# Optimization experiments

Measured on AMD Instinct MI355X. Metric: run time of the kernel, lower is better.

The kernel has to match this reference:

```python
import jax, jax.numpy as jnp
import numpy as np

B, CIN, CMID, COUT, H, W = 4, 64, 128, 128, 128, 128
K = 9  # 3x3 taps
EPS = 1e-5


def conv3x3(x, w, b):
    # standard 3x3 conv, stride 1, pad 1, NCHW / OIHW
    y = jax.lax.conv_general_dilated(x, w, (1, 1), ((1, 1), (1, 1)),
                                     dimension_numbers=('NCHW', 'OIHW', 'NCHW'))
    return y + b[None, :, None, None]


def deform_conv3x3(x, offset, w, b):
    # torchvision DeformConv2d semantics (v1, no mask), kernel 3, pad 1, stride 1.
    # offset: [B, 2*K, H, W] with per-tap (dy, dx) pairs.
    Bn, C, Hn, Wn = x.shape
    off = offset.reshape(Bn, K, 2, Hn, Wn)
    off_y, off_x = off[:, :, 0], off[:, :, 1]          # [B,K,H,W]
    ky = (jnp.arange(K) // 3).astype(x.dtype)          # tap row 0..2
    kx = (jnp.arange(K) % 3).astype(x.dtype)           # tap col 0..2
    # sampling positions: p = out_pos - pad + tap + offset
    py = jnp.arange(Hn, dtype=x.dtype)[None, None, :, None] - 1.0 + ky[None, :, None, None] + off_y
    px = jnp.arange(Wn, dtype=x.dtype)[None, None, None, :] - 1.0 + kx[None, :, None, None] + off_x
    y0 = jnp.floor(py); x0 = jnp.floor(px)
    wy1 = py - y0; wx1 = px - x0                       # bilinear fractions
    y0i = y0.astype(jnp.int32); x0i = x0.astype(jnp.int32)
    xf = x.reshape(Bn, C, Hn * Wn)

    def gather(iy, ix):
        valid = ((iy >= 0) & (iy < Hn) & (ix >= 0) & (ix < Wn)).astype(x.dtype)
        idx = jnp.clip(iy, 0, Hn - 1) * Wn + jnp.clip(ix, 0, Wn - 1)  # [B,K,H,W]
        g = jax.vmap(lambda xb, ib: xb[:, ib])(xf, idx)               # [B,C,K,H,W]
        return g, valid

    g00, v00 = gather(y0i, x0i)
    g01, v01 = gather(y0i, x0i + 1)
    g10, v10 = gather(y0i + 1, x0i)
    g11, v11 = gather(y0i + 1, x0i + 1)

    def wmul(g, v, wgt):
        return g * (v * wgt)[:, None]                  # broadcast over channel dim

    sampled = (wmul(g00, v00, (1 - wy1) * (1 - wx1)) +
               wmul(g01, v01, (1 - wy1) * wx1) +
               wmul(g10, v10, wy1 * (1 - wx1)) +
               wmul(g11, v11, wy1 * wx1))              # [B,C,K,H,W]
    out = jnp.einsum('bckhw,ock->bohw', sampled, w.reshape(w.shape[0], C, K))
    return out + b[None, :, None, None]


def batchnorm_relu(x, gamma, beta):
    # training-mode BN: batch statistics over (N,H,W), biased variance
    mean = jnp.mean(x, axis=(0, 2, 3), keepdims=True)
    var = jnp.mean(jnp.square(x - mean), axis=(0, 2, 3), keepdims=True)
    y = (x - mean) * jax.lax.rsqrt(var + EPS)
    return jax.nn.relu(y * gamma[None, :, None, None] + beta[None, :, None, None])


def setup_inputs() -> dict:
    key = jax.random.key(0)
    ks = jax.random.split(key, 13)
    s = 0.05  # small weights keep offsets small / sampling mostly in-bounds
    return {
        'x': jax.random.normal(ks[0], (B, CIN, H, W), jnp.float32),
        'w_off1': jax.random.normal(ks[1], (2 * K, CIN, 3, 3), jnp.float32) * s,
        'b_off1': jnp.zeros((2 * K,), jnp.float32),
        'w1': jax.random.normal(ks[2], (CMID, CIN, 3, 3), jnp.float32) * s,
        'b1': jax.random.normal(ks[3], (CMID,), jnp.float32) * s,
        'g1': jnp.ones((CMID,), jnp.float32),
        'be1': jnp.zeros((CMID,), jnp.float32),
        'w_off2': jax.random.normal(ks[4], (2 * K, CMID, 3, 3), jnp.float32) * s,
        'b_off2': jnp.zeros((2 * K,), jnp.float32),
        'w2': jax.random.normal(ks[5], (COUT, CMID, 3, 3), jnp.float32) * s,
        'b2': jax.random.normal(ks[6], (COUT,), jnp.float32) * s,
        'g2': jnp.ones((COUT,), jnp.float32),
        'be2': jnp.zeros((COUT,), jnp.float32),
    }


def reference(x, w_off1, b_off1, w1, b1, g1, be1, w_off2, b_off2, w2, b2, g2, be2):
    offset1 = conv3x3(x, w_off1, b_off1)
    out = deform_conv3x3(x, offset1, w1, b1)
    out = batchnorm_relu(out, g1, be1)
    offset2 = conv3x3(out, w_off2, b_off2)
    out = deform_conv3x3(out, offset2, w2, b2)
    out = batchnorm_relu(out, g2, be2)
    return out
```

## Files before the change

kernel.cpp:

```cpp
#include <hip/hip_runtime.h>
#include <hip/hip_bf16.h>

#define BB 4
#define H_ 128
#define W_ 128
#define HWP 16384
#define CIN1 64
#define CMID 128
#define KOFF 18

typedef short short8 __attribute__((ext_vector_type(8)));
typedef float floatx4 __attribute__((ext_vector_type(4)));

#define WS_AB   16
#define WS_CVT  288
#define CVT_TOTAL 4447396
#define WS_WF1  4447744
#define WS_WF2  4484608
#define WS_XT   4558336
#define WS_OFF  6655488
#define WS_Y1   7835136
#define WS_Y1T  16223744
#define WS_OFFB 20418048
#define WS_PART 21600000
#define WS_Y2   WS_Y1

#define R_X     0
#define R_WOFF1 4194304
#define R_BOFF1 4204672
#define R_W1    4204690
#define R_B1    4278418
#define R_G1    4278546
#define R_BE1   4278674
#define R_WOFF2 4278802
#define R_BOFF2 4299538
#define R_W2    4299556
#define R_B2    4447012
#define R_G2    4447140
#define R_BE2   4447268

struct SrcPtrs { const void* p[13]; };

__device__ inline short f2bf(float f) {
    __hip_bfloat16 h = __float2bfloat16(f);
    return *reinterpret_cast<short*>(&h);
}
__device__ inline float bf2f(unsigned short u) {
    return __uint_as_float(((unsigned int)u) << 16);
}
__device__ inline float bfu_lo(unsigned int u) { return __uint_as_float(u << 16); }
__device__ inline float bfu_hi(unsigned int u) { return __uint_as_float(u & 0xFFFF0000u); }
__device__ inline float rl_f(float v, int i) {
    return __int_as_float(__builtin_amdgcn_readlane(__float_as_int(v), i));
}

__global__ void probe_dtype_k(const unsigned int* __restrict__ g1, int* __restrict__ flag) {
    if (threadIdx.x == 0 && blockIdx.x == 0) {
        flag[0] = ((g1[0] & 0xFFFFu) != 0u) ? 1 : 0;
    }
}

__global__ __launch_bounds__(256) void convert_inputs_k(SrcPtrs sp, float* __restrict__ dst,
                                                        const int* __restrict__ flag, int total) {
    int i = blockIdx.x * 256 + threadIdx.x;
    if (i >= total) return;
    constexpr int prefix[13] = {0, R_WOFF1, R_BOFF1, R_W1, R_B1, R_G1, R_BE1,
                                R_WOFF2, R_BOFF2, R_W2, R_B2, R_G2, R_BE2};
    const void* src = sp.p[0];
    int base = 0;
#pragma unroll
    for (int q = 1; q < 13; ++q) {
        if (i >= prefix[q]) { src = sp.p[q]; base = prefix[q]; }
    }
    int local = i - base;
    float v;
    if (flag[0] != 0) {
        v = bf2f(((const unsigned short*)src)[local]);
    } else {
        v = ((const float*)src)[local];
    }
    dst[i] = v;
}

template <int CIN>
__global__ __launch_bounds__(256) void wf_build_k(const float* __restrict__ w, short* __restrict__ wf) {
    constexpr int KSTEPS = CIN * 9 / 32;
    int idx = blockIdx.x * 256 + threadIdx.x;
    int j    = idx & 7;
    int lane = (idx >> 3) & 63;
    int rem  = idx >> 9;
    int ks   = rem % KSTEPS;
    int ct   = rem / KSTEPS;
    int co = ct * 16 + (lane & 15);
    int k  = ks * 32 + (lane >> 4) * 8 + j;
    int ci = k & (CIN - 1);
    int kk = k / CIN;
    wf[idx] = f2bf(w[(co * CIN + ci) * 9 + kk]);
}

__global__ __launch_bounds__(256) void xt_build_k(const float* __restrict__ x, unsigned short* __restrict__ xt) {
    __shared__ __align__(4) short s_t[64 * 66];
    int bi  = blockIdx.x;
    int hw0 = (bi & 255) * 64;
    int b   = bi >> 8;
    int t   = threadIdx.x;
    int hwp = t & 63;
#pragma unroll
    for (int it = 0; it < 16; ++it) {
        int c = it * 4 + (t >> 6);
        float v = x[((long)(b * 64 + c) << 14) + hw0 + hwp];
        s_t[hwp * 66 + c] = f2bf(v);
    }
    __syncthreads();
#pragma unroll
    for (int it = 0; it < 8; ++it) {
        int i  = it * 256 + t;
        int c2 = (i & 31) * 2;
        int hw2 = i >> 5;
        int sv = *(const int*)&s_t[hw2 * 66 + c2];
        *(int*)&xt[((long)((b << 14) + hw0 + hw2)) * 64 + c2] = sv;
    }
}

template <int CIN>
__global__ __launch_bounds__(256) void conv3x3_part_k(const float* __restrict__ x,
                                                      const float* __restrict__ w,
                                                      const float* __restrict__ bias,
                                                      float* __restrict__ outp,
                                                      float* __restrict__ outpb) {
    constexpr int CIQ = CIN / 2;
    int bi = blockIdx.x;
    int h  = bi & 127;
    int b  = (bi >> 7) & 3;
    int q  = bi >> 9;
    int t  = threadIdx.x;
    int wq = t & 127;
    int cg = __builtin_amdgcn_readfirstlane(t >> 7);
    int co0 = cg * 9;
    int ci0 = q * CIQ;

    float acc[9];
#pragma unroll
    for (int j = 0; j < 9; ++j) acc[j] = (q == 0) ? bias[co0 + j] : 0.f;

    const float* xb = x + ((long)(b * CIN + ci0) << 14);
    bool bm = h > 0, bp = h < H_ - 1, bl = wq > 0, br = wq < W_ - 1;
    int rm = (bm ? h - 1 : 0) << 7;
    int rc = h << 7;
    int rp = (bp ? h + 1 : H_ - 1) << 7;

#pragma unroll 2
    for (int ci = 0; ci < CIQ; ++ci) {
        const float* plane = xb + ((long)ci << 14);
        float v0 = plane[rm + wq - 1], v1 = plane[rm + wq], v2 = plane[rm + wq + 1];
        float v3 = plane[rc + wq - 1], v4 = plane[rc + wq], v5 = plane[rc + wq + 1];
        float v6 = plane[rp + wq - 1], v7 = plane[rp + wq], v8 = plane[rp + wq + 1];
        v0 = (bm && bl) ? v0 : 0.f;
        v1 = bm ? v1 : 0.f;
        v2 = (bm && br) ? v2 : 0.f;
        v3 = bl ? v3 : 0.f;
        v5 = br ? v5 : 0.f;
        v6 = (bp && bl) ? v6 : 0.f;
        v7 = bp ? v7 : 0.f;
        v8 = (bp && br) ? v8 : 0.f;
#pragma unroll
        for (int j = 0; j < 9; ++j) {
            const float* wk = w + ((long)(co0 + j) * CIN + ci0 + ci) * 9;
            acc[j] += v0 * wk[0] + v1 * wk[1] + v2 * wk[2]
                    + v3 * wk[3] + v4 * wk[4] + v5 * wk[5]
                    + v6 * wk[6] + v7 * wk[7] + v8 * wk[8];
        }
    }

    float* o = (q == 0) ? outp : outpb;
    long ob = ((long)(b * KOFF + co0) << 14) + (h << 7) + wq;
#pragma unroll
    for (int j = 0; j < 9; ++j) o[ob + ((long)j << 14)] = acc[j];
}

__device__ inline void build_table2(const float* __restrict__ off, const float* __restrict__ offb,
                                    int b, int h, int w0, int lane, int wv,
                                    int& tpk, float& tw0, float& tw1, float& tw2, float& tw3) {
    tpk = 0; tw0 = tw1 = tw2 = tw3 = 0.f;
    if (lane < 36) {
        int r = wv + 8 * lane;
        int p = r & 31;
        int k = r >> 5;
        int wpix = w0 + p;
        long obase = ((long)(b * KOFF) << 14) + (h << 7) + wpix;
        long oyi = obase + ((long)(2 * k) << 14);
        long oxi = obase + ((long)(2 * k + 1) << 14);
        float oy = off[oyi] + offb[oyi];
        float ox = off[oxi] + offb[oxi];
        float py = (float)(h - 1 + (k / 3)) + oy;
        float px = (float)(wpix - 1 + (k % 3)) + ox;
        float fy = floorf(py), fx = floorf(px);
        float wy = py - fy, wx = px - fx;
        int y0 = (int)fy, x0 = (int)fx;
        int y1 = y0 + 1, x1 = x0 + 1;
        bool vy0 = (y0 >= 0) && (y0 < H_);
        bool vy1 = (y1 >= 0) && (y1 < H_);
        bool vx0 = (x0 >= 0) && (x0 < W_);
        bool vx1 = (x1 >= 0) && (x1 < W_);
        float wy0 = 1.f - wy, wx0 = 1.f - wx;
        tw0 = (vy0 && vx0) ? wy0 * wx0 : 0.f;
        tw1 = (vy0 && vx1) ? wy0 * wx  : 0.f;
        tw2 = (vy1 && vx0) ? wy  * wx0 : 0.f;
        tw3 = (vy1 && vx1) ? wy  * wx  : 0.f;
        int iy0 = min(max(y0, 0), H_ - 1), iy1 = min(max(y1, 0), H_ - 1);
        int ix0 = min(max(x0, 0), W_ - 1), ix1 = min(max(x1, 0), W_ - 1);
        int dx = ix1 - ix0;
        int dy = iy1 - iy0;
        tpk = (iy0 * W_ + ix0) | (dx << 14) | (dy << 15);
    }
}

template <int NB>
__device__ inline void gather_batch128v2(const unsigned short* __restrict__ xb, short* __restrict__ s_samp,
                                         int i0, int kkbase, int wv, int lane,
                                         int tpk, float tw0, float tw1, float tw2, float tw3) {
    constexpr int PADc = 648;
    uint4 ub[NB];
#pragma unroll
    for (int j = 0; j < NB; ++j) {
        int pk = __builtin_amdgcn_readlane(tpk, i0 + j);
        const unsigned short* b00 = xb + (pk & 0x3FFF) * 128;
        const unsigned short* b01 = b00 + ((pk >> 14) & 1) * 128;
        const unsigned short* b10 = b00 + ((pk >> 15) & 1) * (W_ * 128);
        const unsigned short* b11 = b01 + ((pk >> 15) & 1) * (W_ * 128);
        ub[j].x = *(const unsigned int*)(b00 + 2 * lane);
        ub[j].y = *(const unsigned int*)(b01 + 2 * lane);
        ub[j].z = *(const unsigned int*)(b10 + 2 * lane);
        ub[j].w = *(const unsigned int*)(b11 + 2 * lane);
    }
#pragma unroll
    for (int j = 0; j < NB; ++j) {
        int i = i0 + j;
        int r = wv + 8 * i;
        float w00 = rl_f(tw0, i), w01 = rl_f(tw1, i), w10 = rl_f(tw2, i), w11 = rl_f(tw3, i);
        float vlo = w00 * bfu_lo(ub[j].x) + w01 * bfu_lo(ub[j].y)
                  + w10 * bfu_lo(ub[j].z) + w11 * bfu_lo(ub[j].w);
        float vhi = w00 * bfu_hi(ub[j].x) + w01 * bfu_hi(ub[j].y)
                  + w10 * bfu_hi(ub[j].z) + w11 * bfu_hi(ub[j].w);
        __hip_bfloat162 h2 = __float22bfloat162_rn(make_float2(vlo, vhi));
        *(unsigned int*)&s_samp[(r & 31) * PADc + ((r >> 5) - kkbase) * 128 + 2 * lane] =
            *reinterpret_cast<unsigned int*>(&h2);
    }
}

template <int NBP>
__device__ inline void gather_batch64v2(const unsigned short* __restrict__ xb, short* __restrict__ s_samp,
                                        int i0, int wv, int half, int li,
                                        int tpk, float tw0, float tw1, float tw2, float tw3) {
    constexpr int PADc = 584;
    uint4 ub[NBP];
#pragma unroll
    for (int j = 0; j < NBP; ++j) {
        int iA = i0 + 2 * j, iB = iA + 1;
        int pkA = __builtin_amdgcn_readlane(tpk, iA);
        int pkB = __builtin_amdgcn_readlane(tpk, iB);
        int pk = half ? pkB : pkA;
        const unsigned short* b00 = xb + (pk & 0x3FFF) * 64;
        const unsigned short* b01 = b00 + ((pk >> 14) & 1) * 64;
        const unsigned short* b10 = b00 + ((pk >> 15) & 1) * (W_ * 64);
        const unsigned short* b11 = b01 + ((pk >> 15) & 1) * (W_ * 64);
        ub[j].x = *(const unsigned int*)(b00 + 2 * li);
        ub[j].y = *(const unsigned int*)(b01 + 2 * li);
        ub[j].z = *(const unsigned int*)(b10 + 2 * li);
        ub[j].w = *(const unsigned int*)(b11 + 2 * li);
    }
#pragma unroll
    for (int j = 0; j < NBP; ++j) {
        int iA = i0 + 2 * j, iB = iA + 1;
        float w00 = half ? rl_f(tw0, iB) : rl_f(tw0, iA);
        float w01 = half ? rl_f(tw1, iB) : rl_f(tw1, iA);
        float w10 = half ? rl_f(tw2, iB) : rl_f(tw2, iA);
        float w11 = half ? rl_f(tw3, iB) : rl_f(tw3, iA);
        float vlo = w00 * bfu_lo(ub[j].x) + w01 * bfu_lo(ub[j].y)
                  + w10 * bfu_lo(ub[j].z) + w11 * bfu_lo(ub[j].w);
        float vhi = w00 * bfu_hi(ub[j].x) + w01 * bfu_hi(ub[j].y)
                  + w10 * bfu_hi(ub[j].z) + w11 * bfu_hi(ub[j].w);
        __hip_bfloat162 h2 = __float22bfloat162_rn(make_float2(vlo, vhi));
        int r = wv + 8 * (half ? iB : iA);
        *(unsigned int*)&s_samp[(r & 31) * PADc + (r >> 5) * 64 + 2 * li] =
            *reinterpret_cast<unsigned int*>(&h2);
    }
}

__global__ __launch_bounds__(512, 4) void deform_mfma64_k(const unsigned short* __restrict__ xt,
                                                          const float* __restrict__ off,
                                                          const float* __restrict__ offb,
                                                          const short* __restrict__ wf,
                                                          const float* __restrict__ bias,
                                                          float* __restrict__ out) {
    constexpr int KSTEPS = 18;
    constexpr int PADc = 584;
    __shared__ __align__(16) short s_samp[32 * PADc];

    int bi = blockIdx.x;
    int w0 = (bi & 3) * 32;
    int h  = (bi >> 2) & 127;
    int b  = bi >> 9;
    int t  = threadIdx.x;
    int lane = t & 63;
    int wv   = t >> 6;

    int tpk; float tw0, tw1, tw2, tw3;
    build_table2(off, offb, b, h, w0, lane, wv, tpk, tw0, tw1, tw2, tw3);
    const unsigned short* xb = xt + (long)b * HWP * 64;
    int half = lane >> 5, li = lane & 31;

    gather_batch64v2<6>(xb, s_samp,  0, wv, half, li, tpk, tw0, tw1, tw2, tw3);
    gather_batch64v2<6>(xb, s_samp, 12, wv, half, li, tpk, tw0, tw1, tw2, tw3);
    gather_batch64v2<6>(xb, s_samp, 24, wv, half, li, tpk, tw0, tw1, tw2, tw3);
    __syncthreads();

    int p_   = lane & 15;
    int quad = lane >> 4;
    int ct = wv;
    floatx4 acc0, acc1;
#pragma unroll
    for (int r = 0; r < 4; ++r) {
        float bv = bias[ct * 16 + quad * 4 + r];
        acc0[r] = bv;
        acc1[r] = bv;
    }
#pragma unroll 3
    for (int ks = 0; ks < KSTEPS; ++ks) {
        short8 a  = *(const short8*)&wf[(((long)ct * KSTEPS + ks) * 64 + lane) * 8];
        short8 b0 = *(const short8*)&s_samp[p_ * PADc + ks * 32 + quad * 8];
        short8 b1 = *(const short8*)&s_samp[(16 + p_) * PADc + ks * 32 + quad * 8];
        acc0 = __builtin_amdgcn_mfma_f32_16x16x32_bf16(a, b0, acc0, 0, 0, 0);
        acc1 = __builtin_amdgcn_mfma_f32_16x16x32_bf16(a, b1, acc1, 0, 0, 0);
    }

    long ob = ((long)(b * 128) << 14) + (h << 7) + w0 + p_;
#pragma unroll
    for (int r = 0; r < 4; ++r) {
        long cpl = (long)(ct * 16 + quad * 4 + r) << 14;
        out[ob + cpl]      = acc0[r];
        out[ob + 16 + cpl] = acc1[r];
    }
}

__global__ __launch_bounds__(512, 4) void deform_mfma128_k(const unsigned short* __restrict__ xt,
                                                           const float* __restrict__ off,
                                                           const float* __restrict__ offb,
                                                           const short* __restrict__ wf,
                                                           const float* __restrict__ bias,
                                                           float* __restrict__ out) {
    constexpr int KSTEPS = 36;
    constexpr int PADc = 648;
    __shared__ __align__(16) short s_samp[32 * PADc];

    int bi = blockIdx.x;
    int w0 = (bi & 3) * 32;
    int h  = (bi >> 2) & 127;
    int b  = bi >> 9;
    int t  = threadIdx.x;
    int lane = t & 63;
    int wv   = t >> 6;

    int tpk; float tw0, tw1, tw2, tw3;
    build_table2(off, offb, b, h, w0, lane, wv, tpk, tw0, tw1, tw2, tw3);
    const unsigned short* xb = xt + (long)b * HWP * 128;

    int p_   = lane & 15;
    int quad = lane >> 4;
    int ct = wv;
    floatx4 acc0, acc1;
#pragma unroll
    for (int r = 0; r < 4; ++r) {
        float bv = bias[ct * 16 + quad * 4 + r];
        acc0[r] = bv;
        acc1[r] = bv;
    }

    gather_batch128v2<8>(xb, s_samp, 0, 0, wv, lane, tpk, tw0, tw1, tw2, tw3);
    gather_batch128v2<8>(xb, s_samp, 8, 0, wv, lane, tpk, tw0, tw1, tw2, tw3);
    __syncthreads();
#pragma unroll 4
    for (int ks = 0; ks < 16; ++ks) {
        short8 a  = *(const short8*)&wf[(((long)ct * KSTEPS + ks) * 64 + lane) * 8];
        short8 b0 = *(const short8*)&s_samp[p_ * PADc + ks * 32 + quad * 8];
        short8 b1 = *(const short8*)&s_samp[(16 + p_) * PADc + ks * 32 + quad * 8];
        acc0 = __builtin_amdgcn_mfma_f32_16x16x32_bf16(a, b0, acc0, 0, 0, 0);
        acc1 = __builtin_amdgcn_mfma_f32_16x16x32_bf16(a, b1, acc1, 0, 0, 0);
    }
    __syncthreads();

    gather_batch128v2<5>(xb, s_samp, 16, 4, wv, lane, tpk, tw0, tw1, tw2, tw3);
    gather_batch128v2<5>(xb, s_samp, 21, 4, wv, lane, tpk, tw0, tw1, tw2, tw3);
    gather_batch128v2<5>(xb, s_samp, 26, 4, wv, lane, tpk, tw0, tw1, tw2, tw3);
    gather_batch128v2<5>(xb, s_samp, 31, 4, wv, lane, tpk, tw0, tw1, tw2, tw3);
    __syncthreads();
#pragma unroll 4
    for (int ks = 16; ks < KSTEPS; ++ks) {
        short8 a  = *(const short8*)&wf[(((long)ct * KSTEPS + ks) * 64 + lane) * 8];
        short8 b0 = *(const short8*)&s_samp[p_ * PADc + (ks - 16) * 32 + quad * 8];
        short8 b1 = *(const short8*)&s_samp[(16 + p_) * PADc + (ks - 16) * 32 + quad * 8];
        acc0 = __builtin_amdgcn_mfma_f32_16x16x32_bf16(a, b0, acc0, 0, 0, 0);
        acc1 = __builtin_amdgcn_mfma_f32_16x16x32_bf16(a, b1, acc1, 0, 0, 0);
    }

    long ob = ((long)(b * 128) << 14) + (h << 7) + w0 + p_;
#pragma unroll
    for (int r = 0; r < 4; ++r) {
        long cpl = (long)(ct * 16 + quad * 4 + r) << 14;
        out[ob + cpl]      = acc0[r];
        out[ob + 16 + cpl] = acc1[r];
    }
}

__global__ __launch_bounds__(256) void bn_stats_part_k(const float* __restrict__ y, float* __restrict__ part) {
    int bi = blockIdx.x;
    int c = bi & 127;
    int b = bi >> 7;
    int t = threadIdx.x;
    const float4* p4 = (const float4*)(y + ((long)(b * 128 + c) << 14));
    float sum = 0.f, ss = 0.f;
#pragma unroll
    for (int i = 0; i < 16; ++i) {
        float4 v = p4[t + 256 * i];
        sum += v.x + v.y + v.z + v.w;
        ss  += v.x * v.x + v.y * v.y + v.z * v.z + v.w * v.w;
    }
#pragma unroll
    for (int o = 32; o > 0; o >>= 1) { sum += __shfl_down(sum, o); ss += __shfl_down(ss, o); }
    __shared__ float s1[4], s2[4];
    int wave = t >> 6;
    if ((t & 63) == 0) { s1[wave] = sum; s2[wave] = ss; }
    __syncthreads();
    if (t == 0) {
        part[bi]       = s1[0] + s1[1] + s1[2] + s1[3];
        part[512 + bi] = s2[0] + s2[1] + s2[2] + s2[3];
    }
}

__global__ __launch_bounds__(256) void bn_apply_dual_k(float* __restrict__ y, const float* __restrict__ part,
                                                       const float* __restrict__ g, const float* __restrict__ be,
                                                       unsigned short* __restrict__ yt) {
    __shared__ __align__(4) short s_t[64 * 134];
    __shared__ float s_a[128], s_sh[128];
    int t = threadIdx.x;
    if (t < 128) {
        float sum = part[t] + part[128 + t] + part[256 + t] + part[384 + t];
        float ss  = part[512 + t] + part[640 + t] + part[768 + t] + part[896 + t];
        float mean = sum * (1.f / 65536.f);
        float var  = ss  * (1.f / 65536.f) - mean * mean;
        float inv  = rsqrtf(var + 1e-5f);
        float a = g[t] * inv;
        s_a[t]  = a;
        s_sh[t] = be[t] - mean * a;
    }
    __syncthreads();

    int bi  = blockIdx.x;
    int hw0 = (bi & 255) * 64;
    int b   = bi >> 8;
    int hwp = t & 63;
#pragma unroll 4
    for (int it = 0; it < 32; ++it) {
        int c = it * 4 + (t >> 6);
        float a = s_a[c], sh = s_sh[c];
        long addr = ((long)(b * 128 + c) << 14) + hw0 + hwp;
        float v = y[addr];
        v = fmaxf(v * a + sh, 0.f);
        y[addr] = v;
        s_t[hwp * 134 + c] = f2bf(v);
    }
    __syncthreads();
#pragma unroll 4
    for (int it = 0; it < 16; ++it) {
        int i   = it * 256 + t;
        int c2  = (i & 63) * 2;
        int hw2 = i >> 6;
        int sv = *(const int*)&s_t[hw2 * 134 + c2];
        *(int*)&yt[((long)((b << 14) + hw0 + hw2)) * 128 + c2] = sv;
    }
}

__global__ __launch_bounds__(256) void bn_apply_out_k(const float* __restrict__ y, const float* __restrict__ part,
                                                      const float* __restrict__ g, const float* __restrict__ be,
                                                      const int* __restrict__ flag, void* __restrict__ out, int total4) {
    __shared__ float s_a[128], s_sh[128];
    int t = threadIdx.x;
    if (t < 128) {
        float sum = part[t] + part[128 + t] + part[256 + t] + part[384 + t];
        float ss  = part[512 + t] + part[640 + t] + part[768 + t] + part[896 + t];
        float mean = sum * (1.f / 65536.f);
        float var  = ss  * (1.f / 65536.f) - mean * mean;
        float inv  = rsqrtf(var + 1e-5f);
        float a = g[t] * inv;
        s_a[t]  = a;
        s_sh[t] = be[t] - mean * a;
    }
    __syncthreads();

    int i = blockIdx.x * 256 + t;
    if (i >= total4) return;
    int c = (i >> 12) & 127;
    float a = s_a[c], sh = s_sh[c];
    float4 v = reinterpret_cast<const float4*>(y)[i];
    v.x = fmaxf(v.x * a + sh, 0.f);
    v.y = fmaxf(v.y * a + sh, 0.f);
    v.z = fmaxf(v.z * a + sh, 0.f);
    v.w = fmaxf(v.w * a + sh, 0.f);
    if (flag[0] != 0) {
        ushort4 u;
        u.x = (unsigned short)f2bf(v.x);
        u.y = (unsigned short)f2bf(v.y);
        u.z = (unsigned short)f2bf(v.z);
        u.w = (unsigned short)f2bf(v.w);
        reinterpret_cast<ushort4*>(out)[i] = u;
    } else {
        reinterpret_cast<float4*>(out)[i] = v;
    }
}

extern "C" void kernel_launch(void* const* d_in, const int* in_sizes, int n_in,
                              void* d_out, int out_size, void* d_ws, size_t ws_size,
                              hipStream_t stream) {
    float* ws   = (float*)d_ws;
    int*   flag = (int*)d_ws;
    float* cvt  = ws + WS_CVT;

    const float* X     = cvt + R_X;
    const float* Woff1 = cvt + R_WOFF1;
    const float* Boff1 = cvt + R_BOFF1;
    const float* W1f   = cvt + R_W1;
    const float* B1f   = cvt + R_B1;
    const float* G1    = cvt + R_G1;
    const float* Be1   = cvt + R_BE1;
    const float* Woff2 = cvt + R_WOFF2;
    const float* Boff2 = cvt + R_BOFF2;
    const float* W2f   = cvt + R_W2;
    const float* B2f   = cvt + R_B2;
    const float* G2    = cvt + R_G2;
    const float* Be2   = cvt + R_BE2;

    short* WF1 = (short*)(ws + WS_WF1);
    short* WF2 = (short*)(ws + WS_WF2);
    unsigned short* XT  = (unsigned short*)(ws + WS_XT);
    unsigned short* Y1T = (unsigned short*)(ws + WS_Y1T);
    float* OFF  = ws + WS_OFF;
    float* OFFB = ws + WS_OFFB;
    float* PART = ws + WS_PART;
    float* Y1   = ws + WS_Y1;
    float* Y2   = ws + WS_Y2;

    SrcPtrs sp;
    for (int j = 0; j < 13; ++j) sp.p[j] = d_in[j];

    probe_dtype_k<<<1, 64, 0, stream>>>((const unsigned int*)d_in[5], flag);
    convert_inputs_k<<<(CVT_TOTAL + 255) / 256, 256, 0, stream>>>(sp, cvt, flag, CVT_TOTAL);
    wf_build_k<64><<<288, 256, 0, stream>>>(W1f, WF1);
    wf_build_k<128><<<576, 256, 0, stream>>>(W2f, WF2);
    xt_build_k<<<1024, 256, 0, stream>>>(X, XT);

    conv3x3_part_k<64><<<BB * 128 * 2, 256, 0, stream>>>(X, Woff1, Boff1, OFF, OFFB);
    deform_mfma64_k<<<BB * 128 * 4, 512, 0, stream>>>(XT, OFF, OFFB, WF1, B1f, Y1);
    bn_stats_part_k<<<512, 256, 0, stream>>>(Y1, PART);
    bn_apply_dual_k<<<1024, 256, 0, stream>>>(Y1, PART, G1, Be1, Y1T);

    conv3x3_part_k<128><<<BB * 128 * 2, 256, 0, stream>>>(Y1, Woff2, Boff2, OFF, OFFB);
    deform_mfma128_k<<<BB * 128 * 4, 512, 0, stream>>>(Y1T, OFF, OFFB, WF2, B2f, Y2);
    bn_stats_part_k<<<512, 256, 0, stream>>>(Y2, PART);
    bn_apply_out_k<<<(BB * 128 * HWP / 4 + 255) / 256, 256, 0, stream>>>(Y2, PART, G2, Be2, flag, d_out, BB * 128 * HWP / 4);
}
```

Measured before the change: 335.2 us.

## Compute offset convolutions with split-bf16 MFMA instead of scalar FP32

Replaces the scalar FP32 direct offset-conv kernels with MFMA kernels that gather 3x3 neighbourhoods from the channel-last bf16 tensors into LDS. Weights and activations are each split into a bf16 hi part and a bf16 lo residual, and three MFMA products (hi*hi, lo*hi, hi*lo) approximate FP32 accuracy. The K reduction is split across waves and combined in LDS, which removes the old partial-sum buffer and the extra load in build_table2. In exchange, the builder kernels must write extra lo-residual tensors, reusing workspace regions whose old contents are assumed dead.

```diff
diff --git a/kernel.cpp b/kernel.cpp
--- a/kernel.cpp
+++ b/kernel.cpp
@@ -21,7 +21,8 @@
 #define WS_OFF  6655488
 #define WS_Y1   7835136
 #define WS_Y1T  16223744
-#define WS_OFFB 20418048
+#define WS_WFO1 20418048
+#define WS_WFO2 20436480
 #define WS_PART 21600000
 #define WS_Y2   WS_Y1
 
@@ -98,8 +99,30 @@
     wf[idx] = f2bf(w[(co * CIN + ci) * 9 + kk]);
 }
 
-__global__ __launch_bounds__(256) void xt_build_k(const float* __restrict__ x, unsigned short* __restrict__ xt) {
+template <int CIN>
+__global__ __launch_bounds__(256) void wf_off_build_k(const float* __restrict__ w, short* __restrict__ wf) {
+    constexpr int KSTEPS = CIN * 9 / 32;
+    int idx = blockIdx.x * 256 + threadIdx.x;
+    int j    = idx & 7;
+    int lane = (idx >> 3) & 63;
+    int rem  = idx >> 9;
+    int ks   = rem % KSTEPS;
+    int cc   = rem / KSTEPS;
+    int sel  = cc >> 1;
+    int co = (cc & 1) * 16 + (lane & 15);
+    int k  = ks * 32 + (lane >> 4) * 8 + j;
+    int ci = k & (CIN - 1);
+    int kk = k / CIN;
+    float v = (co < KOFF) ? w[(co * CIN + ci) * 9 + kk] : 0.f;
+    short hi = f2bf(v);
+    wf[idx] = sel ? f2bf(v - bf2f((unsigned short)hi)) : hi;
+}
+
+__global__ __launch_bounds__(256) void xt_build_k(const float* __restrict__ x,
+                                                  unsigned short* __restrict__ xt,
+                                                  unsigned short* __restrict__ xtl) {
     __shared__ __align__(4) short s_t[64 * 66];
+    __shared__ __align__(4) short s_tl[64 * 66];
     int bi  = blockIdx.x;
     int hw0 = (bi & 255) * 64;
     int b   = bi >> 8;
@@ -109,7 +132,9 @@
     for (int it = 0; it < 16; ++it) {
         int c = it * 4 + (t >> 6);
         float v = x[((long)(b * 64 + c) << 14) + hw0 + hwp];
-        s_t[hwp * 66 + c] = f2bf(v);
+        short hi = f2bf(v);
+        s_t[hwp * 66 + c]  = hi;
+        s_tl[hwp * 66 + c] = f2bf(v - bf2f((unsigned short)hi));
     }
     __syncthreads();
 #pragma unroll
@@ -117,68 +142,242 @@
         int i  = it * 256 + t;
         int c2 = (i & 31) * 2;
         int hw2 = i >> 5;
-        int sv = *(const int*)&s_t[hw2 * 66 + c2];
-        *(int*)&xt[((long)((b << 14) + hw0 + hw2)) * 64 + c2] = sv;
-    }
-}
-
-template <int CIN>
-__global__ __launch_bounds__(256) void conv3x3_part_k(const float* __restrict__ x,
-                                                      const float* __restrict__ w,
-                                                      const float* __restrict__ bias,
-                                                      float* __restrict__ outp,
-                                                      float* __restrict__ outpb) {
-    constexpr int CIQ = CIN / 2;
+        long da = ((long)((b << 14) + hw0 + hw2)) * 64 + c2;
+        *(int*)&xt[da]  = *(const int*)&s_t[hw2 * 66 + c2];
+        *(int*)&xtl[da] = *(const int*)&s_tl[hw2 * 66 + c2];
+    }
+}
+
+__device__ inline int conv_tpk(int h, int w0, int lane, int wv) {
+    int tpk = 0;
+    if (lane < 36) {
+        int r = wv + 8 * lane;
+        int p = r & 31;
+        int k = r >> 5;
+        int y = h - 1 + k / 3;
+        int x = w0 + p - 1 + (k % 3);
+        int valid = (y >= 0 && y < H_ && x >= 0 && x < W_) ? 1 : 0;
+        int yc = min(max(y, 0), H_ - 1), xc = min(max(x, 0), W_ - 1);
+        tpk = (yc * W_ + xc) | (valid << 16);
+    }
+    return tpk;
+}
+
+__device__ inline void convgather64(const unsigned short* __restrict__ xb, short* __restrict__ s_samp,
+                                    int half, int li, int wv, int tpk) {
+    constexpr int PADc = 584;
+    unsigned int ub[18];
+#pragma unroll
+    for (int j = 0; j < 18; ++j) {
+        int pkA = __builtin_amdgcn_readlane(tpk, 2 * j);
+        int pkB = __builtin_amdgcn_readlane(tpk, 2 * j + 1);
+        int pk = half ? pkB : pkA;
+        unsigned int u = *(const unsigned int*)(xb + (pk & 0xFFFF) * 64 + 2 * li);
+        ub[j] = (pk >> 16) ? u : 0u;
+    }
+#pragma unroll
+    for (int j = 0; j < 18; ++j) {
+        int r = wv + 8 * (half ? (2 * j + 1) : (2 * j));
+        *(unsigned int*)&s_samp[(r & 31) * PADc + (r >> 5) * 64 + 2 * li] = ub[j];
+    }
+}
+
+template <int I0, int NJ, int KKB>
+__device__ inline void convgather128(const unsigned short* __restrict__ xb, short* __restrict__ s_samp,
+                                     int lane, int wv, int tpk) {
+    constexpr int PADc = 648;
+    unsigned int ub[NJ];
+#pragma unroll
+    for (int j = 0; j < NJ; ++j) {
+        int pk = __builtin_amdgcn_readlane(tpk, I0 + j);
+        unsigned int u = *(const unsigned int*)(xb + (pk & 0xFFFF) * 128 + 2 * lane);
+        ub[j] = (pk >> 16) ? u : 0u;
+    }
+#pragma unroll
+    for (int j = 0; j < NJ; ++j) {
+        int r = wv + 8 * (I0 + j);
+        *(unsigned int*)&s_samp[(r & 31) * PADc + ((r >> 5) - KKB) * 128 + 2 * lane] = ub[j];
+    }
+}
+
+__global__ __launch_bounds__(512, 4) void conv_off_mfma64_k(const unsigned short* __restrict__ xt,
+                                                            const unsigned short* __restrict__ xtl,
+                                                            const short* __restrict__ wfo,
+                                                            const float* __restrict__ bias,
+                                                            float* __restrict__ off) {
+    constexpr int KSTEPS = 18;
+    constexpr int PADc = 584;
+    __shared__ __align__(16) short s_samp[32 * PADc];
+    __shared__ float s_red[4 * 256];
+
     int bi = blockIdx.x;
-    int h  = bi & 127;
-    int b  = (bi >> 7) & 3;
-    int q  = bi >> 9;
+    int w0 = (bi & 3) * 32;
+    int h  = (bi >> 2) & 127;
+    int b  = bi >> 9;
     int t  = threadIdx.x;
-    int wq = t & 127;
-    int cg = __builtin_amdgcn_readfirstlane(t >> 7);
-    int co0 = cg * 9;
-    int ci0 = q * CIQ;
-
-    float acc[9];
-#pragma unroll
-    for (int j = 0; j < 9; ++j) acc[j] = (q == 0) ? bias[co0 + j] : 0.f;
-
-    const float* xb = x + ((long)(b * CIN + ci0) << 14);
-    bool bm = h > 0, bp = h < H_ - 1, bl = wq > 0, br = wq < W_ - 1;
-    int rm = (bm ? h - 1 : 0) << 7;
-    int rc = h << 7;
-    int rp = (bp ? h + 1 : H_ - 1) << 7;
-
-#pragma unroll 2
-    for (int ci = 0; ci < CIQ; ++ci) {
-        const float* plane = xb + ((long)ci << 14);
-        float v0 = plane[rm + wq - 1], v1 = plane[rm + wq], v2 = plane[rm + wq + 1];
-        float v3 = plane[rc + wq - 1], v4 = plane[rc + wq], v5 = plane[rc + wq + 1];
-        float v6 = plane[rp + wq - 1], v7 = plane[rp + wq], v8 = plane[rp + wq + 1];
-        v0 = (bm && bl) ? v0 : 0.f;
-        v1 = bm ? v1 : 0.f;
-        v2 = (bm && br) ? v2 : 0.f;
-        v3 = bl ? v3 : 0.f;
-        v5 = br ? v5 : 0.f;
-        v6 = (bp && bl) ? v6 : 0.f;
-        v7 = bp ? v7 : 0.f;
-        v8 = (bp && br) ? v8 : 0.f;
-#pragma unroll
-        for (int j = 0; j < 9; ++j) {
-            const float* wk = w + ((long)(co0 + j) * CIN + ci0 + ci) * 9;
-            acc[j] += v0 * wk[0] + v1 * wk[1] + v2 * wk[2]
-                    + v3 * wk[3] + v4 * wk[4] + v5 * wk[5]
-                    + v6 * wk[6] + v7 * wk[7] + v8 * wk[8];
+    int lane = t & 63;
+    int wv   = t >> 6;
+
+    int tpk = conv_tpk(h, w0, lane, wv);
+    const unsigned short* xbh = xt  + (long)b * HWP * 64;
+    const unsigned short* xbl = xtl + (long)b * HWP * 64;
+    int half = lane >> 5, li = lane & 31;
+
+    int p_   = lane & 15;
+    int quad = lane >> 4;
+    int c   = wv & 3;
+    int ksl = wv >> 2;
+    int ct  = c & 1;
+    int pt  = c >> 1;
+    int row = pt * 16 + p_;
+    floatx4 acc;
+#pragma unroll
+    for (int r = 0; r < 4; ++r) {
+        int co = ct * 16 + quad * 4 + r;
+        acc[r] = (ksl == 0 && co < KOFF) ? bias[co] : 0.f;
+    }
+
+    convgather64(xbh, s_samp, half, li, wv, tpk);
+    __syncthreads();
+#pragma unroll
+    for (int ki = 0; ki < 9; ++ki) {
+        int ks = ksl * 9 + ki;
+        short8 bfr = *(const short8*)&s_samp[row * PADc + ks * 32 + quad * 8];
+        short8 ah  = *(const short8*)&wfo[(((long)ct * KSTEPS + ks) * 64 + lane) * 8];
+        short8 al  = *(const short8*)&wfo[(((long)(2 + ct) * KSTEPS + ks) * 64 + lane) * 8];
+        acc = __builtin_amdgcn_mfma_f32_16x16x32_bf16(ah, bfr, acc, 0, 0, 0);
+        acc = __builtin_amdgcn_mfma_f32_16x16x32_bf16(al, bfr, acc, 0, 0, 0);
+    }
+    __syncthreads();
+
+    convgather64(xbl, s_samp, half, li, wv, tpk);
+    __syncthreads();
+#pragma unroll
+    for (int ki = 0; ki < 9; ++ki) {
+        int ks = ksl * 9 + ki;
+        short8 bfr = *(const short8*)&s_samp[row * PADc + ks * 32 + quad * 8];
+        short8 ah  = *(const short8*)&wfo[(((long)ct * KSTEPS + ks) * 64 + lane) * 8];
+        acc = __builtin_amdgcn_mfma_f32_16x16x32_bf16(ah, bfr, acc, 0, 0, 0);
+    }
+
+    if (ksl == 1) {
+#pragma unroll
+        for (int r = 0; r < 4; ++r) s_red[c * 256 + (quad * 4 + r) * 16 + p_] = acc[r];
+    }
+    __syncthreads();
+    if (ksl == 0) {
+#pragma unroll
+        for (int r = 0; r < 4; ++r) {
+            int co = ct * 16 + quad * 4 + r;
+            if (co < KOFF) {
+                float v = acc[r] + s_red[c * 256 + (quad * 4 + r) * 16 + p_];
+                off[((long)(b * KOFF + co) << 14) + (h << 7) + w0 + pt * 16 + p_] = v;
+            }
         }
     }
-
-    float* o = (q == 0) ? outp : outpb;
-    long ob = ((long)(b * KOFF + co0) << 14) + (h << 7) + wq;
-#pragma unroll
-    for (int j = 0; j < 9; ++j) o[ob + ((long)j << 14)] = acc[j];
-}
-
-__device__ inline void build_table2(const float* __restrict__ off, const float* __restrict__ offb,
+}
+
+__global__ __launch_bounds__(512, 4) void conv_off_mfma128_k(const unsigned short* __restrict__ xt,
+                                                             const unsigned short* __restrict__ xtl,
+                                                             const short* __restrict__ wfo,
+                                                             const float* __restrict__ bias,
+                                                             float* __restrict__ off) {
+    constexpr int KSTEPS = 36;
+    constexpr int PADc = 648;
+    __shared__ __align__(16) short s_samp[32 * PADc];
+    __shared__ float s_red[4 * 256];
+
+    int bi = blockIdx.x;
+    int w0 = (bi & 3) * 32;
+    int h  = (bi >> 2) & 127;
+    int b  = bi >> 9;
+    int t  = threadIdx.x;
+    int lane = t & 63;
+    int wv   = t >> 6;
+
+    int tpk = conv_tpk(h, w0, lane, wv);
+    const unsigned short* xbh = xt  + (long)b * HWP * 128;
+    const unsigned short* xbl = xtl + (long)b * HWP * 128;
+
+    int p_   = lane & 15;
+    int quad = lane >> 4;
+    int c   = wv & 3;
+    int ksl = wv >> 2;
+    int ct  = c & 1;
+    int pt  = c >> 1;
+    int row = pt * 16 + p_;
+    floatx4 acc;
+#pragma unroll
+    for (int r = 0; r < 4; ++r) {
+        int co = ct * 16 + quad * 4 + r;
+        acc[r] = (ksl == 0 && co < KOFF) ? bias[co] : 0.f;
+    }
+
+    convgather128<0, 16, 0>(xbh, s_samp, lane, wv, tpk);
+    __syncthreads();
+#pragma unroll
+    for (int ki = 0; ki < 8; ++ki) {
+        int ks = ksl * 8 + ki;
+        short8 bfr = *(const short8*)&s_samp[row * PADc + ks * 32 + quad * 8];
+        short8 ah  = *(const short8*)&wfo[(((long)ct * KSTEPS + ks) * 64 + lane) * 8];
+        short8 al  = *(const short8*)&wfo[(((long)(2 + ct) * KSTEPS + ks) * 64 + lane) * 8];
+        acc = __builtin_amdgcn_mfma_f32_16x16x32_bf16(ah, bfr, acc, 0, 0, 0);
+        acc = __builtin_amdgcn_mfma_f32_16x16x32_bf16(al, bfr, acc, 0, 0, 0);
+    }
+    __syncthreads();
+
+    convgather128<16, 20, 4>(xbh, s_samp, lane, wv, tpk);
+    __syncthreads();
+#pragma unroll
+    for (int ki = 0; ki < 10; ++ki) {
+        int ks = 16 + ksl * 10 + ki;
+        short8 bfr = *(const short8*)&s_samp[row * PADc + (ks - 16) * 32 + quad * 8];
+        short8 ah  = *(const short8*)&wfo[(((long)ct * KSTEPS + ks) * 64 + lane) * 8];
+        short8 al  = *(const short8*)&wfo[(((long)(2 + ct) * KSTEPS + ks) * 64 + lane) * 8];
+        acc = __builtin_amdgcn_mfma_f32_16x16x32_bf16(ah, bfr, acc, 0, 0, 0);
+        acc = __builtin_amdgcn_mfma_f32_16x16x32_bf16(al, bfr, acc, 0, 0, 0);
+    }
+    __syncthreads();
+
+    convgather128<0, 16, 0>(xbl, s_samp, lane, wv, tpk);
+    __syncthreads();
+#pragma unroll
+    for (int ki = 0; ki < 8; ++ki) {
+        int ks = ksl * 8 + ki;
+        short8 bfr = *(const short8*)&s_samp[row * PADc + ks * 32 + quad * 8];
+        short8 ah  = *(const short8*)&wfo[(((long)ct * KSTEPS + ks) * 64 + lane) * 8];
+        acc = __builtin_amdgcn_mfma_f32_16x16x32_bf16(ah, bfr, acc, 0, 0, 0);
+    }
+    __syncthreads();
+
+    convgather128<16, 20, 4>(xbl, s_samp, lane, wv, tpk);
+    __syncthreads();
+#pragma unroll
+    for (int ki = 0; ki < 10; ++ki) {
+        int ks = 16 + ksl * 10 + ki;
+        short8 bfr = *(const short8*)&s_samp[row * PADc + (ks - 16) * 32 + quad * 8];
+        short8 ah  = *(const short8*)&wfo[(((long)ct * KSTEPS + ks) * 64 + lane) * 8];
+        acc = __builtin_amdgcn_mfma_f32_16x16x32_bf16(ah, bfr, acc, 0, 0, 0);
+    }
+
+    if (ksl == 1) {
+#pragma unroll
+        for (int r = 0; r < 4; ++r) s_red[c * 256 + (quad * 4 + r) * 16 + p_] = acc[r];
+    }
+    __syncthreads();
+    if (ksl == 0) {
+#pragma unroll
+        for (int r = 0; r < 4; ++r) {
+            int co = ct * 16 + quad * 4 + r;
+            if (co < KOFF) {
+                float v = acc[r] + s_red[c * 256 + (quad * 4 + r) * 16 + p_];
+                off[((long)(b * KOFF + co) << 14) + (h << 7) + w0 + pt * 16 + p_] = v;
+            }
+        }
+    }
+}
+
+__device__ inline void build_table2(const float* __restrict__ off,
                                     int b, int h, int w0, int lane, int wv,
                                     int& tpk, float& tw0, float& tw1, float& tw2, float& tw3) {
     tpk = 0; tw0 = tw1 = tw2 = tw3 = 0.f;
@@ -188,10 +387,8 @@
         int k = r >> 5;
         int wpix = w0 + p;
         long obase = ((long)(b * KOFF) << 14) + (h << 7) + wpix;
-        long oyi = obase + ((long)(2 * k) << 14);
-        long oxi = obase + ((long)(2 * k + 1) << 14);
-        float oy = off[oyi] + offb[oyi];
-        float ox = off[oxi] + offb[oxi];
+        float oy = off[obase + ((long)(2 * k) << 14)];
+        float ox = off[obase + ((long)(2 * k + 1) << 14)];
         float py = (float)(h - 1 + (k / 3)) + oy;
         float px = (float)(wpix - 1 + (k % 3)) + ox;
         float fy = floorf(py), fx = floorf(px);
@@ -289,7 +486,6 @@
 
 __global__ __launch_bounds__(512, 4) void deform_mfma64_k(const unsigned short* __restrict__ xt,
                                                           const float* __restrict__ off,
-                                                          const float* __restrict__ offb,
                                                           const short* __restrict__ wf,
                                                           const float* __restrict__ bias,
                                                           float* __restrict__ out) {
@@ -306,7 +502,7 @@
     int wv   = t >> 6;
 
     int tpk; float tw0, tw1, tw2, tw3;
-    build_table2(off, offb, b, h, w0, lane, wv, tpk, tw0, tw1, tw2, tw3);
+    build_table2(off, b, h, w0, lane, wv, tpk, tw0, tw1, tw2, tw3);
     const unsigned short* xb = xt + (long)b * HWP * 64;
     int half = lane >> 5, li = lane & 31;
 
@@ -345,7 +541,6 @@
 
 __global__ __launch_bounds__(512, 4) void deform_mfma128_k(const unsigned short* __restrict__ xt,
                                                            const float* __restrict__ off,
-                                                           const float* __restrict__ offb,
                                                            const short* __restrict__ wf,
                                                            const float* __restrict__ bias,
                                                            float* __restrict__ out) {
@@ -362,7 +557,7 @@
     int wv   = t >> 6;
 
     int tpk; float tw0, tw1, tw2, tw3;
-    build_table2(off, offb, b, h, w0, lane, wv, tpk, tw0, tw1, tw2, tw3);
+    build_table2(off, b, h, w0, lane, wv, tpk, tw0, tw1, tw2, tw3);
     const unsigned short* xb = xt + (long)b * HWP * 128;
 
     int p_   = lane & 15;
@@ -439,8 +634,10 @@
 
 __global__ __launch_bounds__(256) void bn_apply_dual_k(float* __restrict__ y, const float* __restrict__ part,
                                                        const float* __restrict__ g, const float* __restrict__ be,
-                                                       unsigned short* __restrict__ yt) {
+                                                       unsigned short* __restrict__ yt,
+                                                       unsigned short* __restrict__ ytl) {
     __shared__ __align__(4) short s_t[64 * 134];
+    __shared__ __align__(4) short s_tl[64 * 134];
     __shared__ float s_a[128], s_sh[128];
     int t = threadIdx.x;
     if (t < 128) {
@@ -467,7 +664,9 @@
         float v = y[addr];
         v = fmaxf(v * a + sh, 0.f);
         y[addr] = v;
-        s_t[hwp * 134 + c] = f2bf(v);
+        short hi = f2bf(v);
+        s_t[hwp * 134 + c]  = hi;
+        s_tl[hwp * 134 + c] = f2bf(v - bf2f((unsigned short)hi));
     }
     __syncthreads();
 #pragma unroll 4
@@ -475,8 +674,9 @@
         int i   = it * 256 + t;
         int c2  = (i & 63) * 2;
         int hw2 = i >> 6;
-        int sv = *(const int*)&s_t[hw2 * 134 + c2];
-        *(int*)&yt[((long)((b << 14) + hw0 + hw2)) * 128 + c2] = sv;
+        long da = ((long)((b << 14) + hw0 + hw2)) * 128 + c2;
+        *(int*)&yt[da]  = *(const int*)&s_t[hw2 * 134 + c2];
+        *(int*)&ytl[da] = *(const int*)&s_tl[hw2 * 134 + c2];
     }
 }
 
@@ -539,12 +739,15 @@
     const float* G2    = cvt + R_G2;
     const float* Be2   = cvt + R_BE2;
 
-    short* WF1 = (short*)(ws + WS_WF1);
-    short* WF2 = (short*)(ws + WS_WF2);
-    unsigned short* XT  = (unsigned short*)(ws + WS_XT);
-    unsigned short* Y1T = (unsigned short*)(ws + WS_Y1T);
+    short* WF1  = (short*)(ws + WS_WF1);
+    short* WF2  = (short*)(ws + WS_WF2);
+    short* WFO1 = (short*)(ws + WS_WFO1);
+    short* WFO2 = (short*)(ws + WS_WFO2);
+    unsigned short* XT   = (unsigned short*)(ws + WS_XT);
+    unsigned short* XTL  = (unsigned short*)(ws + WS_Y1);
+    unsigned short* Y1T  = (unsigned short*)(ws + WS_Y1T);
+    unsigned short* Y1TL = (unsigned short*)(ws + WS_CVT);
     float* OFF  = ws + WS_OFF;
-    float* OFFB = ws + WS_OFFB;
     float* PART = ws + WS_PART;
     float* Y1   = ws + WS_Y1;
     float* Y2   = ws + WS_Y2;
@@ -556,15 +759,17 @@
     convert_inputs_k<<<(CVT_TOTAL + 255) / 256, 256, 0, stream>>>(sp, cvt, flag, CVT_TOTAL);
     wf_build_k<64><<<288, 256, 0, stream>>>(W1f, WF1);
     wf_build_k<128><<<576, 256, 0, stream>>>(W2f, WF2);
-    xt_build_k<<<1024, 256, 0, stream>>>(X, XT);
-
-    conv3x3_part_k<64><<<BB * 128 * 2, 256, 0, stream>>>(X, Woff1, Boff1, OFF, OFFB);
-    deform_mfma64_k<<<BB * 128 * 4, 512, 0, stream>>>(XT, OFF, OFFB, WF1, B1f, Y1);
+    wf_off_build_k<64><<<144, 256, 0, stream>>>(Woff1, WFO1);
+    wf_off_build_k<128><<<288, 256, 0, stream>>>(Woff2, WFO2);
+    xt_build_k<<<1024, 256, 0, stream>>>(X, XT, XTL);
+
+    conv_off_mfma64_k<<<BB * 128 * 4, 512, 0, stream>>>(XT, XTL, WFO1, Boff1, OFF);
+    deform_mfma64_k<<<BB * 128 * 4, 512, 0, stream>>>(XT, OFF, WF1, B1f, Y1);
     bn_stats_part_k<<<512, 256, 0, stream>>>(Y1, PART);
-    bn_apply_dual_k<<<1024, 256, 0, stream>>>(Y1, PART, G1, Be1, Y1T);
-
-    conv3x3_part_k<128><<<BB * 128 * 2, 256, 0, stream>>>(Y1, Woff2, Boff2, OFF, OFFB);
-    deform_mfma128_k<<<BB * 128 * 4, 512, 0, stream>>>(Y1T, OFF, OFFB, WF2, B2f, Y2);
+    bn_apply_dual_k<<<1024, 256, 0, stream>>>(Y1, PART, G1, Be1, Y1T, Y1TL);
+
+    conv_off_mfma128_k<<<BB * 128 * 4, 512, 0, stream>>>(Y1T, Y1TL, WFO2, Boff2, OFF);
+    deform_mfma128_k<<<BB * 128 * 4, 512, 0, stream>>>(Y1T, OFF, WF2, B2f, Y2);
     bn_stats_part_k<<<512, 256, 0, stream>>>(Y2, PART);
     bn_apply_out_k<<<(BB * 128 * HWP / 4 + 255) / 256, 256, 0, stream>>>(Y2, PART, G2, Be2, flag, d_out, BB * 128 * HWP / 4);
 }
```

After: 343.2 us. 2.4% more time.
